# Kernel optimization log

Hardware: AMD Instinct MI355X
Metric: run time of the kernel (lower is better)

The kernel has to match this reference:

```python
import jax, jax.numpy as jnp
import numpy as np

# Modulated deformable conv2d (torchvision semantics): per kernel tap, sample the
# input at a runtime-offset location via bilinear interpolation (zero padding
# outside the image), modulate with mask, then do the weighted accumulation.

STRIDE = (1, 1)
PADDING = (1, 1)
DILATION = (1, 1)


def deform_conv2d(x, offset, mask, weight, bias):
    B, C, H, W = x.shape
    O, Cg, kh, kw = weight.shape
    K = kh * kw
    og = offset.shape[1] // (2 * K)          # offset groups
    Ho, Wo = offset.shape[2], offset.shape[3]
    sh, sw = STRIDE
    ph, pw = PADDING
    dh, dw = DILATION

    off = offset.reshape(B, og, K, 2, Ho, Wo)
    ki = jnp.arange(K)
    base_ky = ((ki // kw) * dh).astype(x.dtype)            # [K]
    base_kx = ((ki % kw) * dw).astype(x.dtype)
    base_h = (jnp.arange(Ho) * sh - ph).astype(x.dtype)    # [Ho]
    base_w = (jnp.arange(Wo) * sw - pw).astype(x.dtype)    # [Wo]
    # sampling positions, [B, og, K, Ho, Wo]
    p_y = off[:, :, :, 0] + base_ky[None, None, :, None, None] + base_h[None, None, None, :, None]
    p_x = off[:, :, :, 1] + base_kx[None, None, :, None, None] + base_w[None, None, None, None, :]

    y0 = jnp.floor(p_y)
    x0 = jnp.floor(p_x)
    ly = p_y - y0
    lx = p_x - x0
    y0i = y0.astype(jnp.int32)
    x0i = x0.astype(jnp.int32)

    Cog = C // og
    x_flat = x.reshape(B, og, Cog, H * W)

    def gather(yi, xi):
        valid = ((yi >= 0) & (yi < H) & (xi >= 0) & (xi < W))
        idx = jnp.clip(yi, 0, H - 1) * W + jnp.clip(xi, 0, W - 1)
        idx_flat = idx.reshape(B, og, 1, K * Ho * Wo)
        v = jnp.take_along_axis(x_flat, idx_flat, axis=3).reshape(B, og, Cog, K, Ho, Wo)
        return v * valid[:, :, None].astype(x.dtype)

    w00 = ((1 - ly) * (1 - lx))[:, :, None]
    w01 = ((1 - ly) * lx)[:, :, None]
    w10 = (ly * (1 - lx))[:, :, None]
    w11 = (ly * lx)[:, :, None]
    val = (w00 * gather(y0i, x0i) + w01 * gather(y0i, x0i + 1)
           + w10 * gather(y0i + 1, x0i) + w11 * gather(y0i + 1, x0i + 1))

    if mask is not None:
        val = val * mask.reshape(B, og, K, Ho, Wo)[:, :, None]

    # grouped conv accumulation over sampled taps
    G = C // Cg                               # conv groups (=1 here)
    val = val.reshape(B, G, C // G, K, Ho, Wo)
    w = weight.reshape(G, O // G, Cg, K)
    out = jnp.einsum('bgckhw,gock->bgohw', val, w).reshape(B, O, Ho, Wo)
    if bias is not None:
        out = out + bias[None, :, None, None]
    return out


def setup_inputs() -> dict:
    key = jax.random.key(0)
    k1, k2, k3, k4, k5 = jax.random.split(key, 5)
    B, C, H, W = 4, 64, 128, 128
    O, kh, kw = 64, 3, 3
    return {
        'input': jax.random.normal(k1, (B, C, H, W), dtype=jnp.float32),
        'offset': jax.random.normal(k2, (B, 2 * kh * kw, H, W), dtype=jnp.float32),
        'mask': jax.random.uniform(k3, (B, kh * kw, H, W), dtype=jnp.float32),
        'weight': jax.random.normal(k4, (O, C, kh, kw), dtype=jnp.float32) * (1.0 / np.sqrt(C * kh * kw)),
        'bias': jax.random.normal(k5, (O,), dtype=jnp.float32) * 0.01,
    }


def reference(input, offset, mask, weight, bias):
    return deform_conv2d(input, offset, mask, weight, bias)
```

## Files before the change

kernel.cpp:

```cpp
#include <hip/hip_runtime.h>


#define BB 4
#define CC 64
#define HH 128
#define WW 128
#define OO 64
#define KHW 3
#define KK 9
#define HW (HH * WW)

typedef __bf16 bf16_t;
typedef bf16_t bf16x8 __attribute__((ext_vector_type(8)));
typedef float f32x4 __attribute__((ext_vector_type(4)));

__global__ __launch_bounds__(256) void nhwc_kernel(const float* __restrict__ x,
                                                   bf16_t* __restrict__ xt) {
    __shared__ float tile[64 * 65];
    const int t  = threadIdx.x;
    const int b  = blockIdx.x >> 8;
    const int p0 = (blockIdx.x & 255) << 6;
#pragma unroll
    for (int i = 0; i < 16; ++i) {
        int c = i * 4 + (t >> 6);
        int p = t & 63;
        tile[c * 65 + p] = x[(b * CC + c) * HW + p0 + p];
    }
    __syncthreads();
#pragma unroll
    for (int i = 0; i < 16; ++i) {
        int p = i * 4 + (t >> 6);
        int c = t & 63;
        xt[(size_t)((b * HW) + p0 + p) * CC + c] = (bf16_t)tile[c * 65 + p];
    }
}

__global__ void wfrag_kernel(const float* __restrict__ w,
                             bf16_t* __restrict__ wf) {
    int i = blockIdx.x * blockDim.x + threadIdx.x;
    if (i >= OO * CC * KK) return;
    int j    = i & 7;
    int lane = (i >> 3) & 63;
    int nt   = (i >> 9) & 3;
    int q    = (i >> 11) & 1;
    int k    = i >> 12;
    int o = nt * 16 + (lane & 15);
    int c = q * 32 + ((lane >> 4) << 3) + j;
    wf[i] = (bf16_t)w[(o * CC + c) * KK + k];
}

__global__ __launch_bounds__(256) void deform_conv_mfma(
    const bf16_t* __restrict__ xt, const float* __restrict__ offset,
    const float* __restrict__ mask, const bf16x8* __restrict__ wf,
    const float* __restrict__ bias, float* __restrict__ out) {
    const int t       = threadIdx.x;
    const int b       = blockIdx.x >> 8;
    const int p0      = (blockIdx.x & 255) << 6;
    const int p_local = t >> 2;
    const int c0      = (t & 3) << 4;
    const int rem     = p0 + p_local;
    const int ho      = rem >> 7;
    const int wo      = rem & (WW - 1);
    const int lane    = t & 63;
    const int wv      = t >> 6;
    const int m0      = wv << 4;
    const int col     = lane & 15;
    const int quad    = lane >> 4;

    __shared__ bf16_t V[2][64][72];

    const bf16_t* xb = xt + (size_t)b * HW * CC;

    f32x4 acc[4];
#pragma unroll
    for (int nt = 0; nt < 4; ++nt) acc[nt] = (f32x4){0.f, 0.f, 0.f, 0.f};

    for (int k = 0; k < KK; ++k) {
        float offy = offset[((b * (2 * KK) + 2 * k) * HW) + rem];
        float offx = offset[((b * (2 * KK) + 2 * k + 1) * HW) + rem];
        float mm   = mask[((b * KK + k) * HW) + rem];
        float py = offy + (float)(k / KHW) + (float)(ho - 1);
        float px = offx + (float)(k % KHW) + (float)(wo - 1);
        float fy0 = floorf(py), fx0 = floorf(px);
        float ly = py - fy0, lx = px - fx0;
        int y0 = (int)fy0, x0 = (int)fx0;
        int y1 = y0 + 1, x1 = x0 + 1;
        bool vy0 = (y0 >= 0) && (y0 < HH);
        bool vy1 = (y1 >= 0) && (y1 < HH);
        bool vx0 = (x0 >= 0) && (x0 < WW);
        bool vx1 = (x1 >= 0) && (x1 < WW);
        int cy0 = min(max(y0, 0), HH - 1), cy1 = min(max(y1, 0), HH - 1);
        int cx0 = min(max(x0, 0), WW - 1), cx1 = min(max(x1, 0), WW - 1);
        float w0 = (vy0 && vx0) ? mm * (1.0f - ly) * (1.0f - lx) : 0.0f;
        float w1 = (vy0 && vx1) ? mm * (1.0f - ly) * lx : 0.0f;
        float w2 = (vy1 && vx0) ? mm * ly * (1.0f - lx) : 0.0f;
        float w3 = (vy1 && vx1) ? mm * ly * lx : 0.0f;

        const bf16x8* A0 = (const bf16x8*)(xb + (cy0 * WW + cx0) * CC + c0);
        const bf16x8* A1 = (const bf16x8*)(xb + (cy0 * WW + cx1) * CC + c0);
        const bf16x8* A2 = (const bf16x8*)(xb + (cy1 * WW + cx0) * CC + c0);
        const bf16x8* A3 = (const bf16x8*)(xb + (cy1 * WW + cx1) * CC + c0);
        bf16x8 a0l = A0[0], a0h = A0[1];
        bf16x8 a1l = A1[0], a1h = A1[1];
        bf16x8 a2l = A2[0], a2h = A2[1];
        bf16x8 a3l = A3[0], a3h = A3[1];

        bf16x8 r0, r1;
#pragma unroll
        for (int i = 0; i < 8; ++i) {
            float v = w0 * (float)a0l[i] + w1 * (float)a1l[i] +
                      w2 * (float)a2l[i] + w3 * (float)a3l[i];
            r0[i] = (bf16_t)v;
        }
#pragma unroll
        for (int i = 0; i < 8; ++i) {
            float v = w0 * (float)a0h[i] + w1 * (float)a1h[i] +
                      w2 * (float)a2h[i] + w3 * (float)a3h[i];
            r1[i] = (bf16_t)v;
        }
        const int buf = k & 1;
        *(bf16x8*)(&V[buf][p_local][c0])     = r0;
        *(bf16x8*)(&V[buf][p_local][c0 + 8]) = r1;

        __syncthreads();

#pragma unroll
        for (int q = 0; q < 2; ++q) {
            bf16x8 af = *(const bf16x8*)(&V[buf][m0 + col][q * 32 + quad * 8]);
#pragma unroll
            for (int nt = 0; nt < 4; ++nt) {
                bf16x8 bfg = wf[((k * 2 + q) * 4 + nt) * 64 + lane];
                acc[nt] = __builtin_amdgcn_mfma_f32_16x16x32_bf16(
                    af, bfg, acc[nt], 0, 0, 0);
            }
        }
    }

#pragma unroll
    for (int nt = 0; nt < 4; ++nt) {
        int o = nt * 16 + col;
        float bv = bias[o];
        f32x4 r = acc[nt];
        r.x += bv; r.y += bv; r.z += bv; r.w += bv;
        float* dst = out + (size_t)(b * OO + o) * HW + p0 + m0 + quad * 4;
        *(f32x4*)dst = r;
    }
}

extern "C" void kernel_launch(void* const* d_in, const int* in_sizes, int n_in,
                              void* d_out, int out_size, void* d_ws,
                              size_t ws_size, hipStream_t stream) {
    const float* x      = (const float*)d_in[0];
    const float* offset = (const float*)d_in[1];
    const float* mask   = (const float*)d_in[2];
    const float* weight = (const float*)d_in[3];
    const float* bias   = (const float*)d_in[4];
    float* out = (float*)d_out;

    bf16_t* xt = (bf16_t*)d_ws;
    bf16_t* wfr = (bf16_t*)((char*)d_ws + (size_t)BB * HW * CC * 2);

    nhwc_kernel<<<BB * (HW / 64), 256, 0, stream>>>(x, xt);

    int nw = OO * CC * KK;
    wfrag_kernel<<<(nw + 255) / 256, 256, 0, stream>>>(weight, wfr);

    deform_conv_mfma<<<BB * (HW / 64), 256, 0, stream>>>(
        xt, offset, mask, (const bf16x8*)wfr, bias, out);
}
```

Before: 114.9 us.

## Build MFMA A-fragments directly in registers, removing LDS staging and barriers

Each lane now gathers and bilinearly blends the exact 8-channel slices its MFMA A-fragment needs (pixel m0+col, channels quad*8 and quad*8+32), so the shared-memory tile and the per-tap __syncthreads are removed. Every wave now works on its own 16 pixels with no block-level synchronisation. In exchange, each lane computes sampling coordinates redundantly for four quads and gathers two 16-byte chunks 64 bytes apart instead of a contiguous 32 bytes. Launch bounds also request at least two blocks per SIMD-level occupancy.

```diff
diff --git a/kernel.cpp b/kernel.cpp
--- a/kernel.cpp
+++ b/kernel.cpp
@@ -49,25 +49,23 @@
     wf[i] = (bf16_t)w[(o * CC + c) * KK + k];
 }
 
-__global__ __launch_bounds__(256) void deform_conv_mfma(
+__global__ __launch_bounds__(256, 2) void deform_conv_mfma(
     const bf16_t* __restrict__ xt, const float* __restrict__ offset,
     const float* __restrict__ mask, const bf16x8* __restrict__ wf,
     const float* __restrict__ bias, float* __restrict__ out) {
-    const int t       = threadIdx.x;
-    const int b       = blockIdx.x >> 8;
-    const int p0      = (blockIdx.x & 255) << 6;
-    const int p_local = t >> 2;
-    const int c0      = (t & 3) << 4;
-    const int rem     = p0 + p_local;
-    const int ho      = rem >> 7;
-    const int wo      = rem & (WW - 1);
-    const int lane    = t & 63;
-    const int wv      = t >> 6;
-    const int m0      = wv << 4;
-    const int col     = lane & 15;
-    const int quad    = lane >> 4;
+    const int t    = threadIdx.x;
+    const int b    = blockIdx.x >> 8;
+    const int p0   = (blockIdx.x & 255) << 6;
+    const int lane = t & 63;
+    const int wv   = t >> 6;
+    const int m0   = wv << 4;
+    const int col  = lane & 15;
+    const int quad = lane >> 4;
 
-    __shared__ bf16_t V[2][64][72];
+    const int rem = p0 + m0 + col;
+    const int ho  = rem >> 7;
+    const int wo  = rem & (WW - 1);
+    const int chq = quad << 3;
 
     const bf16_t* xb = xt + (size_t)b * HW * CC;
 
@@ -96,43 +94,46 @@
         float w2 = (vy1 && vx0) ? mm * ly * (1.0f - lx) : 0.0f;
         float w3 = (vy1 && vx1) ? mm * ly * lx : 0.0f;
 
-        const bf16x8* A0 = (const bf16x8*)(xb + (cy0 * WW + cx0) * CC + c0);
-        const bf16x8* A1 = (const bf16x8*)(xb + (cy0 * WW + cx1) * CC + c0);
-        const bf16x8* A2 = (const bf16x8*)(xb + (cy1 * WW + cx0) * CC + c0);
-        const bf16x8* A3 = (const bf16x8*)(xb + (cy1 * WW + cx1) * CC + c0);
-        bf16x8 a0l = A0[0], a0h = A0[1];
-        bf16x8 a1l = A1[0], a1h = A1[1];
-        bf16x8 a2l = A2[0], a2h = A2[1];
-        bf16x8 a3l = A3[0], a3h = A3[1];
+        const bf16_t* c00 = xb + (cy0 * WW + cx0) * CC + chq;
+        const bf16_t* c01 = xb + (cy0 * WW + cx1) * CC + chq;
+        const bf16_t* c10 = xb + (cy1 * WW + cx0) * CC + chq;
+        const bf16_t* c11 = xb + (cy1 * WW + cx1) * CC + chq;
 
-        bf16x8 r0, r1;
+        bf16x8 a00 = *(const bf16x8*)(c00);
+        bf16x8 a01 = *(const bf16x8*)(c01);
+        bf16x8 a02 = *(const bf16x8*)(c10);
+        bf16x8 a03 = *(const bf16x8*)(c11);
+        bf16x8 a10 = *(const bf16x8*)(c00 + 32);
+        bf16x8 a11 = *(const bf16x8*)(c01 + 32);
+        bf16x8 a12 = *(const bf16x8*)(c10 + 32);
+        bf16x8 a13 = *(const bf16x8*)(c11 + 32);
+
+        bf16x8 af0, af1;
 #pragma unroll
         for (int i = 0; i < 8; ++i) {
-            float v = w0 * (float)a0l[i] + w1 * (float)a1l[i] +
-                      w2 * (float)a2l[i] + w3 * (float)a3l[i];
-            r0[i] = (bf16_t)v;
+            float v = w0 * (float)a00[i] + w1 * (float)a01[i] +
+                      w2 * (float)a02[i] + w3 * (float)a03[i];
+            af0[i] = (bf16_t)v;
         }
 #pragma unroll
         for (int i = 0; i < 8; ++i) {
-            float v = w0 * (float)a0h[i] + w1 * (float)a1h[i] +
-                      w2 * (float)a2h[i] + w3 * (float)a3h[i];
-            r1[i] = (bf16_t)v;
+            float v = w0 * (float)a10[i] + w1 * (float)a11[i] +
+                      w2 * (float)a12[i] + w3 * (float)a13[i];
+            af1[i] = (bf16_t)v;
         }
-        const int buf = k & 1;
-        *(bf16x8*)(&V[buf][p_local][c0])     = r0;
-        *(bf16x8*)(&V[buf][p_local][c0 + 8]) = r1;
 
-        __syncthreads();
-
+        const bf16x8* wk = wf + (size_t)(k * 8) * 64;
 #pragma unroll
-        for (int q = 0; q < 2; ++q) {
-            bf16x8 af = *(const bf16x8*)(&V[buf][m0 + col][q * 32 + quad * 8]);
+        for (int nt = 0; nt < 4; ++nt) {
+            bf16x8 b0 = wk[nt * 64 + lane];
+            acc[nt] = __builtin_amdgcn_mfma_f32_16x16x32_bf16(af0, b0, acc[nt],
+                                                              0, 0, 0);
+        }
 #pragma unroll
-            for (int nt = 0; nt < 4; ++nt) {
-                bf16x8 bfg = wf[((k * 2 + q) * 4 + nt) * 64 + lane];
-                acc[nt] = __builtin_amdgcn_mfma_f32_16x16x32_bf16(
-                    af, bfg, acc[nt], 0, 0, 0);
-            }
+        for (int nt = 0; nt < 4; ++nt) {
+            bf16x8 b1 = wk[(4 + nt) * 64 + lane];
+            acc[nt] = __builtin_amdgcn_mfma_f32_16x16x32_bf16(af1, b1, acc[nt],
+                                                              0, 0, 0);
         }
     }
 
@@ -157,7 +158,7 @@
     const float* bias   = (const float*)d_in[4];
     float* out = (float*)d_out;
 
-    bf16_t* xt = (bf16_t*)d_ws;
+    bf16_t* xt  = (bf16_t*)d_ws;
     bf16_t* wfr = (bf16_t*)((char*)d_ws + (size_t)BB * HW * CC * 2);
 
     nhwc_kernel<<<BB * (HW / 64), 256, 0, stream>>>(x, xt);
```

Result: slower. 124.0 us (+7.9%).
